# Kernel tuning notes

Measured on AMD Instinct MI355X. Metric: run time of the kernel, lower is better.

The kernel has to match this reference:

```python
import jax, jax.numpy as jnp
import numpy as np

# Production-scale dims (GraspNet-style CloudCrop)
B, N, C, NS = 8, 1024, 256, 32          # batch, seed points (= npoint), feat dim, nsample
RADIUS, HMIN, HMAX = 0.05, -0.02, 0.04
EPS = 1e-5


def setup_inputs() -> dict:
    key = jax.random.key(0)
    ks = jax.random.split(key, 8)
    # seed points in a 0.2m cube -> cylinder of r=0.05, h=0.06 holds ~60 pts on avg
    seed_xyz_graspable = jax.random.uniform(ks[0], (B, N, 3), dtype=jnp.float32) * 0.2
    seed_features_graspable = jax.random.normal(ks[1], (B, C, N), dtype=jnp.float32)
    # random proper-ish rotation matrices via batched QR (orthonormal columns)
    q, _ = jnp.linalg.qr(jax.random.normal(ks[2], (B, N, 3, 3), dtype=jnp.float32))
    vp_rot = q
    cin = 3 + C
    # kaiming_normal for 1x1 convs (fan_in = cin), BN -> no conv bias
    W1 = jax.random.normal(ks[3], (256, cin), dtype=jnp.float32) * np.sqrt(2.0 / cin)
    W2 = jax.random.normal(ks[4], (256, 256), dtype=jnp.float32) * np.sqrt(2.0 / 256)
    g1 = jnp.ones((256,), jnp.float32); b1 = jnp.zeros((256,), jnp.float32)
    g2 = jnp.ones((256,), jnp.float32); b2 = jnp.zeros((256,), jnp.float32)
    return dict(seed_xyz_graspable=seed_xyz_graspable,
                seed_features_graspable=seed_features_graspable,
                vp_rot=vp_rot, W1=W1, g1=g1, b1=b1, W2=W2, g2=g2, b2=b2)


def _cylinder_query_idx(xyz, new_xyz, rot):
    # local coords: x_rot = R^T (p - c); rot flattened row-major in the original,
    # so local_k = sum_m rot[m, k] * diff_m  ==  einsum(diff, rot)
    diff = xyz[:, None, :, :] - new_xyz[:, :, None, :]          # (B, P, N, 3)
    local = jnp.einsum('bpnm,bpmk->bpnk', diff, rot)            # (B, P, N, 3)
    d2 = local[..., 1] ** 2 + local[..., 2] ** 2
    mask = (d2 < RADIUS ** 2) & (local[..., 0] > HMIN) & (local[..., 0] < HMAX)
    # first NS in-cylinder indices in original point order; empty slots -> index 0
    order = jnp.argsort(~mask, axis=-1)[..., :NS]               # stable sort
    valid = jnp.take_along_axis(mask, order, axis=-1)
    return jnp.where(valid, order, 0)                           # (B, P, NS) int32


def _conv_bn_relu(x, W, g, b):
    # 1x1 conv as channel GEMM, BatchNorm2d (training stats), ReLU
    y = jnp.einsum('bcps,oc->bops', x, W)                       # (B, O, P, S)
    mu = y.mean(axis=(0, 2, 3), keepdims=True)
    var = y.var(axis=(0, 2, 3), keepdims=True)
    y = (y - mu) * jax.lax.rsqrt(var + EPS)
    y = y * g[None, :, None, None] + b[None, :, None, None]
    return jax.nn.relu(y)


def reference(seed_xyz_graspable, seed_features_graspable, vp_rot,
              W1, g1, b1, W2, g2, b2):
    xyz, feats, rot = seed_xyz_graspable, seed_features_graspable, vp_rot
    idx = _cylinder_query_idx(xyz, xyz, rot)                    # centers == seeds
    # group xyz: gather, recenter, normalize by radius, rotate into cylinder frame
    gx = jax.vmap(lambda p, i: p[i])(xyz, idx)                  # (B, P, NS, 3)
    gx = (gx - xyz[:, :, None, :]) / RADIUS
    gx = jnp.einsum('bpsm,bpmk->bpsk', gx, rot)                 # rotate_xyz
    gf = jax.vmap(lambda f, i: f[:, i])(feats, idx)             # (B, C, P, NS)
    x = jnp.concatenate([gx.transpose(0, 3, 1, 2), gf], axis=1)  # (B, 3+C, P, NS)
    x = _conv_bn_relu(x, W1, g1, b1)
    x = _conv_bn_relu(x, W2, g2, b2)
    return x.max(axis=-1)                                        # (B, 256, P)
```

## Files before the change

kernel.cpp:

```cpp
#include <hip/hip_runtime.h>
#include <hip/hip_bf16.h>

#define DB 8
#define DN 1024
#define DP 1024
#define DC 256
#define DNS 32
#define DBP (DB * DP)
#define K1 288
#define K2 256
#define XS 296
#define YS 258
#define ROWS 128
#define NG (DBP / 4)
#define NK1 (K1 / 32)
#define NK2 (K2 / 32)

constexpr float kRadius = 0.05f;
constexpr float kR2 = kRadius * kRadius;
constexpr float kHmin = -0.02f;
constexpr float kHmax = 0.04f;
constexpr float kEps = 1e-5f;
constexpr float kInvCnt = 1.0f / (float)(DB * DP * DNS);

typedef __bf16 bf16x8 __attribute__((ext_vector_type(8)));
typedef float f32x4 __attribute__((ext_vector_type(4)));
static_assert(sizeof(bf16x8) == 16, "bf16x8 must be 16B");
static_assert(ROWS * XS >= ROWS * YS, "y tile must fit in x_lds");

constexpr size_t OF_FEATST = 0;
constexpr size_t OF_W1B  = OF_FEATST + (size_t)DB * DN * DC / 2;
constexpr size_t OF_W2B  = OF_W1B + (size_t)DC * K1 / 2;
constexpr size_t OF_IDX  = OF_W2B + (size_t)DC * K2 / 2;
constexpr size_t OF_GX   = OF_IDX + (size_t)DBP * DNS;
constexpr size_t OF_PART = OF_GX + (size_t)DBP * DNS * 3;
constexpr size_t OF_YMAX = OF_PART + (size_t)DBP * DC * 2;
constexpr size_t OF_YMIN = OF_YMAX + (size_t)DBP * DC;
constexpr size_t OF_BN1  = OF_YMIN + (size_t)DBP * DC;
constexpr size_t OF_BN2  = OF_BN1 + 512;

__device__ inline ushort f2b(float x) {
  union { __hip_bfloat16 h; ushort u; } c;
  c.h = __float2bfloat16(x);
  return c.u;
}
__device__ inline float b2f(ushort u) {
  union { uint u; float f; } c;
  c.u = (uint)u << 16;
  return c.f;
}

__global__ void k_transpose_feats(const float* __restrict__ f, uint* __restrict__ ftb) {
  __shared__ float t[32][33];
  int ct = blockIdx.x, nt = blockIdx.y, b = blockIdx.z;
  int tx = threadIdx.x, ty = threadIdx.y;
#pragma unroll
  for (int k = 0; k < 4; ++k) {
    int c = ct * 32 + ty + k * 8;
    t[ty + k * 8][tx] = f[((size_t)b * DC + c) * DN + nt * 32 + tx];
  }
  __syncthreads();
  int tid = ty * 32 + tx;
  uint* dst = ftb + (size_t)b * DN * (DC / 2);
#pragma unroll
  for (int it = 0; it < 2; ++it) {
    int idx = it * 256 + tid;
    int nl = idx >> 4, cp = idx & 15;
    uint v = (uint)f2b(t[2 * cp][nl]) | ((uint)f2b(t[2 * cp + 1][nl]) << 16);
    dst[(size_t)(nt * 32 + nl) * (DC / 2) + ct * 16 + cp] = v;
  }
}

__global__ void k_prep_w1(const float* __restrict__ W1, ushort* __restrict__ W1b) {
  int gid = blockIdx.x * 256 + threadIdx.x;
  if (gid >= DC * K1) return;
  int o = gid / K1, kp = gid - o * K1;
  float v = 0.f;
  if (kp < 256) v = W1[o * 259 + 3 + kp];
  else if (kp < 259) v = W1[o * 259 + (kp - 256)];
  W1b[gid] = f2b(v);
}

__global__ void k_prep_w2(const float* __restrict__ W2, ushort* __restrict__ W2b) {
  int gid = blockIdx.x * 256 + threadIdx.x;
  if (gid >= DC * K2) return;
  W2b[gid] = f2b(W2[gid]);
}

__global__ void k_query(const float* __restrict__ xyz, const float* __restrict__ rot,
                        int* __restrict__ idxp, float* __restrict__ gxp) {
  int bp = blockIdx.x;
  int b = bp >> 10;
  int lane = threadIdx.x;
  __shared__ int sidx[DNS];
  __shared__ float srot[9], sc[3];
  if (lane < DNS) sidx[lane] = 0;
  if (lane < 9) srot[lane] = rot[(size_t)bp * 9 + lane];
  if (lane < 3) sc[lane] = xyz[(size_t)bp * 3 + lane];
  __syncthreads();
  float r00 = srot[0], r01 = srot[1], r02 = srot[2];
  float r10 = srot[3], r11 = srot[4], r12 = srot[5];
  float r20 = srot[6], r21 = srot[7], r22 = srot[8];
  float cx = sc[0], cy = sc[1], cz = sc[2];
  const float* xb = xyz + (size_t)b * DN * 3;
  int cnt = 0;
  for (int ch = 0; ch < DN / 64 && cnt < DNS; ++ch) {
    int n = ch * 64 + lane;
    float dx = xb[n * 3 + 0] - cx, dy = xb[n * 3 + 1] - cy, dz = xb[n * 3 + 2] - cz;
    float lx = dx * r00 + dy * r10 + dz * r20;
    float ly = dx * r01 + dy * r11 + dz * r21;
    float lz = dx * r02 + dy * r12 + dz * r22;
    bool m = (ly * ly + lz * lz < kR2) && (lx > kHmin) && (lx < kHmax);
    unsigned long long bal = __ballot(m);
    int rank = cnt + __popcll(bal & ((1ull << lane) - 1ull));
    if (m && rank < DNS) sidx[rank] = n;
    cnt += __popcll(bal);
  }
  __syncthreads();
  if (lane < DNS) {
    int j = sidx[lane];
    idxp[(size_t)bp * DNS + lane] = j;
    float gx = (xb[j * 3 + 0] - cx) / kRadius;
    float gy = (xb[j * 3 + 1] - cy) / kRadius;
    float gz = (xb[j * 3 + 2] - cz) / kRadius;
    float* gp = gxp + ((size_t)bp * DNS + lane) * 3;
    gp[0] = gx * r00 + gy * r10 + gz * r20;
    gp[1] = gx * r01 + gy * r11 + gz * r21;
    gp[2] = gx * r02 + gy * r12 + gz * r22;
  }
}

template <bool FULL>
__global__ __launch_bounds__(256, 2)
void k_gemm(const uint4* __restrict__ ftb, const ushort* __restrict__ W1b,
            const ushort* __restrict__ W2b, const int* __restrict__ idxp,
            const float* __restrict__ gxp, const float* __restrict__ bn1,
            float2* __restrict__ part, float* __restrict__ ymax,
            float* __restrict__ ymin) {
  __shared__ ushort x_lds[ROWS * XS];
  __shared__ float bn_lds[2 * DC];

  const int grp = blockIdx.x;
  const int bp0 = grp * 4;
  const int b = bp0 >> 10;
  const int tid = threadIdx.x;
  const int lane = tid & 63;
  const int wv = tid >> 6;
  const int l15 = lane & 15;
  const int l4 = lane >> 4;

  if constexpr (FULL) {
    for (int i = tid; i < 2 * DC; i += 256) bn_lds[i] = bn1[i];
  }

  {
    int q = tid & 7;
#pragma unroll
    for (int rep = 0; rep < 4; ++rep) {
      int s = (tid >> 3) + rep * 32;
      int j = idxp[(size_t)bp0 * DNS + s];
      const uint4* src = ftb + (size_t)(b * DN + j) * (DC / 8);
      uint4* dst = (uint4*)(x_lds + (size_t)s * XS);
#pragma unroll
      for (int k = 0; k < 4; ++k) dst[q + 8 * k] = src[q + 8 * k];
    }
  }
  if (tid < ROWS) {
    const float* g = gxp + ((size_t)bp0 * DNS + tid) * 3;
    uint a0 = (uint)f2b(g[0]) | ((uint)f2b(g[1]) << 16);
    uint a1 = (uint)f2b(g[2]);
    uint4* drow = (uint4*)(x_lds + (size_t)tid * XS + 256);
    drow[0] = make_uint4(a0, a1, 0u, 0u);
    drow[1] = make_uint4(0u, 0u, 0u, 0u);
    drow[2] = make_uint4(0u, 0u, 0u, 0u);
    drow[3] = make_uint4(0u, 0u, 0u, 0u);
  }
  __syncthreads();

  f32x4 acc[4][8];
#pragma unroll
  for (int t = 0; t < 4; ++t)
#pragma unroll
    for (int st = 0; st < 8; ++st)
#pragma unroll
      for (int r = 0; r < 4; ++r) acc[t][st][r] = 0.f;

  const int o0 = wv * 64;
  const ushort* xbase = x_lds + (size_t)l15 * XS + l4 * 8;

  {
    const ushort* wrow[4];
#pragma unroll
    for (int t = 0; t < 4; ++t)
      wrow[t] = W1b + (size_t)(o0 + t * 16 + l15) * K1 + l4 * 8;
    bf16x8 aw[4];
#pragma unroll
    for (int t = 0; t < 4; ++t) aw[t] = *(const bf16x8*)(wrow[t]);
#pragma unroll
    for (int ks = 0; ks < NK1; ++ks) {
      bf16x8 bx[8];
#pragma unroll
      for (int st = 0; st < 8; ++st)
        bx[st] = *(const bf16x8*)(xbase + (size_t)st * 16 * XS + ks * 32);
      bf16x8 an[4];
      if (ks + 1 < NK1) {
#pragma unroll
        for (int t = 0; t < 4; ++t)
          an[t] = *(const bf16x8*)(wrow[t] + (ks + 1) * 32);
      }
#pragma unroll
      for (int st = 0; st < 8; ++st)
#pragma unroll
        for (int t = 0; t < 4; ++t)
          acc[t][st] = __builtin_amdgcn_mfma_f32_16x16x32_bf16(aw[t], bx[st],
                                                               acc[t][st], 0, 0, 0);
      if (ks + 1 < NK1) {
#pragma unroll
        for (int t = 0; t < 4; ++t) aw[t] = an[t];
      }
    }
  }

  if constexpr (!FULL) {
    __syncthreads();
#pragma unroll
    for (int t = 0; t < 4; ++t) {
      int ob = o0 + t * 16 + l4 * 4;
#pragma unroll
      for (int st = 0; st < 8; ++st) {
        uint2 pk = make_uint2(
            (uint)f2b(acc[t][st][0]) | ((uint)f2b(acc[t][st][1]) << 16),
            (uint)f2b(acc[t][st][2]) | ((uint)f2b(acc[t][st][3]) << 16));
        int s = st * 16 + l15;
        *(uint2*)(x_lds + (size_t)s * YS + ob) = pk;
      }
    }
    __syncthreads();
    {
      const ushort* col = x_lds + tid;
      float s = 0.f, q = 0.f;
#pragma unroll 8
      for (int i = 0; i < ROWS; ++i) {
        float v = b2f(col[(size_t)i * YS]);
        s += v; q += v * v;
      }
      part[(size_t)grp * DC + tid] = make_float2(s, q);
    }
  } else {
    __syncthreads();
#pragma unroll
    for (int t = 0; t < 4; ++t) {
      int ob = o0 + t * 16 + l4 * 4;
      float sc0 = bn_lds[ob + 0], sh0 = bn_lds[DC + ob + 0];
      float sc1 = bn_lds[ob + 1], sh1 = bn_lds[DC + ob + 1];
      float sc2 = bn_lds[ob + 2], sh2 = bn_lds[DC + ob + 2];
      float sc3 = bn_lds[ob + 3], sh3 = bn_lds[DC + ob + 3];
#pragma unroll
      for (int st = 0; st < 8; ++st) {
        float v0 = fmaxf(fmaf(acc[t][st][0], sc0, sh0), 0.f);
        float v1 = fmaxf(fmaf(acc[t][st][1], sc1, sh1), 0.f);
        float v2 = fmaxf(fmaf(acc[t][st][2], sc2, sh2), 0.f);
        float v3 = fmaxf(fmaf(acc[t][st][3], sc3, sh3), 0.f);
        uint2 pk = make_uint2((uint)f2b(v0) | ((uint)f2b(v1) << 16),
                              (uint)f2b(v2) | ((uint)f2b(v3) << 16));
        int s = st * 16 + l15;
        *(uint2*)(x_lds + (size_t)s * XS + ob) = pk;
        acc[t][st][0] = 0.f; acc[t][st][1] = 0.f;
        acc[t][st][2] = 0.f; acc[t][st][3] = 0.f;
      }
    }
    __syncthreads();

    {
      const ushort* wrow[4];
#pragma unroll
      for (int t = 0; t < 4; ++t)
        wrow[t] = W2b + (size_t)(o0 + t * 16 + l15) * K2 + l4 * 8;
      bf16x8 aw[4];
#pragma unroll
      for (int t = 0; t < 4; ++t) aw[t] = *(const bf16x8*)(wrow[t]);
#pragma unroll
      for (int ks = 0; ks < NK2; ++ks) {
        bf16x8 bx[8];
#pragma unroll
        for (int st = 0; st < 8; ++st)
          bx[st] = *(const bf16x8*)(xbase + (size_t)st * 16 * XS + ks * 32);
        bf16x8 an[4];
        if (ks + 1 < NK2) {
#pragma unroll
          for (int t = 0; t < 4; ++t)
            an[t] = *(const bf16x8*)(wrow[t] + (ks + 1) * 32);
        }
#pragma unroll
        for (int st = 0; st < 8; ++st)
#pragma unroll
          for (int t = 0; t < 4; ++t)
            acc[t][st] = __builtin_amdgcn_mfma_f32_16x16x32_bf16(aw[t], bx[st],
                                                                 acc[t][st], 0, 0, 0);
        if (ks + 1 < NK2) {
#pragma unroll
          for (int t = 0; t < 4; ++t) aw[t] = an[t];
        }
      }
    }

    __syncthreads();
#pragma unroll
    for (int t = 0; t < 4; ++t) {
      int ob = o0 + t * 16 + l4 * 4;
#pragma unroll
      for (int st = 0; st < 8; ++st) {
        uint2 pk = make_uint2(
            (uint)f2b(acc[t][st][0]) | ((uint)f2b(acc[t][st][1]) << 16),
            (uint)f2b(acc[t][st][2]) | ((uint)f2b(acc[t][st][3]) << 16));
        int s = st * 16 + l15;
        *(uint2*)(x_lds + (size_t)s * YS + ob) = pk;
      }
    }
    __syncthreads();
    {
      const ushort* col = x_lds + tid;
      float s = 0.f, q = 0.f;
#pragma unroll
      for (int p = 0; p < 4; ++p) {
        float mx = -3.4e38f, mn = 3.4e38f;
#pragma unroll 8
        for (int i = 0; i < DNS; ++i) {
          float v = b2f(col[(size_t)(p * DNS + i) * YS]);
          s += v; q += v * v;
          mx = fmaxf(mx, v); mn = fminf(mn, v);
        }
        ymax[(size_t)(bp0 + p) * DC + tid] = mx;
        ymin[(size_t)(bp0 + p) * DC + tid] = mn;
      }
      part[(size_t)grp * DC + tid] = make_float2(s, q);
    }
  }
}

__global__ void k_reduce_bn(const float* __restrict__ part, const float* __restrict__ gam,
                            const float* __restrict__ bet, float* __restrict__ bn) {
  int o = blockIdx.x, tid = threadIdx.x;
  __shared__ float ss[256], sq[256];
  float s = 0.f, q = 0.f;
  const float2* pp = (const float2*)part;
  for (int g = tid; g < NG; g += 256) {
    float2 v = pp[(size_t)g * DC + o];
    s += v.x; q += v.y;
  }
  ss[tid] = s; sq[tid] = q;
  __syncthreads();
  for (int w = 128; w > 0; w >>= 1) {
    if (tid < w) { ss[tid] += ss[tid + w]; sq[tid] += sq[tid + w]; }
    __syncthreads();
  }
  if (tid == 0) {
    float mu = ss[0] * kInvCnt;
    float var = sq[0] * kInvCnt - mu * mu;
    var = var < 0.f ? 0.f : var;
    float sc = gam[o] * rsqrtf(var + kEps);
    bn[o] = sc;
    bn[DC + o] = bet[o] - mu * sc;
  }
}

__global__ void k_final(const float* __restrict__ ymax, const float* __restrict__ ymin,
                        const float* __restrict__ bn2, float* __restrict__ out) {
  __shared__ float tmax[32][33], tmin[32][33];
  int ot = blockIdx.x, pt = blockIdx.y, b = blockIdx.z;
  int tx = threadIdx.x, ty = threadIdx.y;
#pragma unroll
  for (int k = 0; k < 4; ++k) {
    int pr = ty + k * 8;
    size_t base = ((size_t)(b * DP) + pt * 32 + pr) * DC + ot * 32 + tx;
    tmax[pr][tx] = ymax[base];
    tmin[pr][tx] = ymin[base];
  }
  __syncthreads();
#pragma unroll
  for (int k = 0; k < 4; ++k) {
    int oc = ty + k * 8;
    int o = ot * 32 + oc;
    float sc = bn2[o], sh = bn2[DC + o];
    float m = (sc >= 0.f) ? tmax[tx][oc] : tmin[tx][oc];
    float v = fmaf(sc, m, sh);
    v = v > 0.f ? v : 0.f;
    out[((size_t)(b * DC) + o) * DP + pt * 32 + tx] = v;
  }
}

extern "C" void kernel_launch(void* const* d_in, const int* in_sizes, int n_in,
                              void* d_out, int out_size, void* d_ws, size_t ws_size,
                              hipStream_t stream) {
  const float* xyz   = (const float*)d_in[0];
  const float* feats = (const float*)d_in[1];
  const float* rot   = (const float*)d_in[2];
  const float* W1    = (const float*)d_in[3];
  const float* g1    = (const float*)d_in[4];
  const float* b1    = (const float*)d_in[5];
  const float* W2    = (const float*)d_in[6];
  const float* g2    = (const float*)d_in[7];
  const float* b2    = (const float*)d_in[8];
  float* out = (float*)d_out;

  float* ws = (float*)d_ws;
  uint*   ftb_u  = (uint*)(ws + OF_FEATST);
  uint4*  ftb    = (uint4*)(ws + OF_FEATST);
  ushort* W1b    = (ushort*)(ws + OF_W1B);
  ushort* W2b    = (ushort*)(ws + OF_W2B);
  int*    idxp   = (int*)(ws + OF_IDX);
  float*  gxp    = ws + OF_GX;
  float2* partp  = (float2*)(ws + OF_PART);
  float*  ymaxp  = ws + OF_YMAX;
  float*  yminp  = ws + OF_YMIN;
  float*  bn1p   = ws + OF_BN1;
  float*  bn2p   = ws + OF_BN2;

  k_transpose_feats<<<dim3(DC / 32, DN / 32, DB), dim3(32, 8), 0, stream>>>(feats, ftb_u);
  k_prep_w1<<<(DC * K1 + 255) / 256, 256, 0, stream>>>(W1, W1b);
  k_prep_w2<<<(DC * K2 + 255) / 256, 256, 0, stream>>>(W2, W2b);
  k_query<<<DBP, 64, 0, stream>>>(xyz, rot, idxp, gxp);

  k_gemm<false><<<NG, 256, 0, stream>>>(ftb, W1b, W2b, idxp, gxp, bn1p, partp,
                                        ymaxp, yminp);
  k_reduce_bn<<<DC, 256, 0, stream>>>((const float*)partp, g1, b1, bn1p);
  k_gemm<true><<<NG, 256, 0, stream>>>(ftb, W1b, W2b, idxp, gxp, bn1p, partp,
                                       ymaxp, yminp);
  k_reduce_bn<<<DC, 256, 0, stream>>>((const float*)partp, g2, b2, bn2p);
  k_final<<<dim3(DC / 32, DP / 32, DB), dim3(32, 8), 0, stream>>>(ymaxp, yminp, bn2p, out);
}
```

Before: 169.6 us.

## Compute BN1 statistics analytically from weighted feature Gram matrix instead of GEMM pass

Replaces the first full gathered GEMM pass, which existed only to gather BN1 sum and sum-of-squares, with an algebraic route. Per-point gather counts and summed local xyz are built with atomics, then a count-weighted second-moment matrix of the input channels is formed. BN1 mean and variance follow from W1 times that matrix times W1 transposed. This removes a whole pass of gather, MFMA and reduction over all 262k samples, at the cost of several small kernels, atomics and fp32 variance-by-subtraction precision risk.

```diff
diff --git a/kernel.cpp b/kernel.cpp
--- a/kernel.cpp
+++ b/kernel.cpp
@@ -26,7 +26,6 @@
 typedef __bf16 bf16x8 __attribute__((ext_vector_type(8)));
 typedef float f32x4 __attribute__((ext_vector_type(4)));
 static_assert(sizeof(bf16x8) == 16, "bf16x8 must be 16B");
-static_assert(ROWS * XS >= ROWS * YS, "y tile must fit in x_lds");
 
 constexpr size_t OF_FEATST = 0;
 constexpr size_t OF_W1B  = OF_FEATST + (size_t)DB * DN * DC / 2;
@@ -38,6 +37,11 @@
 constexpr size_t OF_YMIN = OF_YMAX + (size_t)DBP * DC;
 constexpr size_t OF_BN1  = OF_YMIN + (size_t)DBP * DC;
 constexpr size_t OF_BN2  = OF_BN1 + 512;
+constexpr size_t OF_CNT  = OF_BN2 + 512;
+constexpr size_t OF_GW   = OF_CNT + (size_t)DB * DN;
+constexpr size_t OF_GG   = OF_GW + (size_t)DB * 3 * DN;
+constexpr size_t OF_CM   = OF_GG + 16;
+constexpr int    ZN      = DB * DN + DB * 3 * DN + 16 + 257 * 259;
 
 __device__ inline ushort f2b(float x) {
   union { __hip_bfloat16 h; ushort u; } c;
@@ -130,13 +134,158 @@
   }
 }
 
-template <bool FULL>
+__global__ void k_zero(float* __restrict__ p, int n) {
+  int i = blockIdx.x * 256 + threadIdx.x;
+  if (i < n) p[i] = 0.f;
+}
+
+__global__ __launch_bounds__(256)
+void k_count(const int* __restrict__ idxp, const float* __restrict__ gxp,
+             float* __restrict__ cnt, float* __restrict__ gw, float* __restrict__ gg) {
+  int t = threadIdx.x;
+  float p[6] = {0.f, 0.f, 0.f, 0.f, 0.f, 0.f};
+#pragma unroll
+  for (int r = 0; r < 4; ++r) {
+    int sid = blockIdx.x * 1024 + r * 256 + t;
+    int b = sid >> 15;
+    int j = idxp[sid];
+    const float* g = gxp + (size_t)sid * 3;
+    float g0 = g[0], g1 = g[1], g2 = g[2];
+    atomicAdd(&cnt[b * DN + j], 1.f);
+    atomicAdd(&gw[(b * 3 + 0) * DN + j], g0);
+    atomicAdd(&gw[(b * 3 + 1) * DN + j], g1);
+    atomicAdd(&gw[(b * 3 + 2) * DN + j], g2);
+    p[0] += g0 * g0; p[1] += g0 * g1; p[2] += g0 * g2;
+    p[3] += g1 * g1; p[4] += g1 * g2; p[5] += g2 * g2;
+  }
+  __shared__ float sgg[4][6];
+#pragma unroll
+  for (int v = 0; v < 6; ++v) {
+    float s = p[v];
+#pragma unroll
+    for (int m = 1; m < 64; m <<= 1) s += __shfl_xor(s, m, 64);
+    if ((t & 63) == 0) sgg[t >> 6][v] = s;
+  }
+  __syncthreads();
+  if (t < 6) {
+    float s = sgg[0][t] + sgg[1][t] + sgg[2][t] + sgg[3][t];
+    const int i1[6] = {0, 1, 2, 4, 5, 8};
+    const int i2[6] = {0, 3, 6, 4, 7, 8};
+    atomicAdd(&gg[i1[t]], s);
+    if (i2[t] != i1[t]) atomicAdd(&gg[i2[t]], s);
+  }
+}
+
+__global__ __launch_bounds__(256)
+void k_xxt(const float* __restrict__ feats, const float* __restrict__ cnt,
+           const float* __restrict__ gw, float* __restrict__ Cm) {
+  __shared__ float As[16][65], Bs[16][65];
+  int bt = blockIdx.z >> 2;
+  int n0 = (blockIdx.z & 3) * 256;
+  int r0 = blockIdx.x * 64, c0 = blockIdx.y * 64;
+  int tid = threadIdx.x;
+  int ty = tid >> 4, tx = tid & 15;
+  int li = tid >> 2, lq = tid & 3;
+  const float* fb = feats + (size_t)bt * DC * DN;
+  const float* cb = cnt + (size_t)bt * DN;
+  const float* gb = gw + (size_t)bt * 3 * DN;
+  float acc[4][4];
+#pragma unroll
+  for (int u = 0; u < 4; ++u)
+#pragma unroll
+    for (int v = 0; v < 4; ++v) acc[u][v] = 0.f;
+
+  for (int nc = n0; nc < n0 + 256; nc += 16) {
+    __syncthreads();
+    {
+      int k1 = r0 + li;
+      float4 av = make_float4(0.f, 0.f, 0.f, 0.f);
+      if (k1 < 256) av = *(const float4*)(fb + (size_t)k1 * DN + nc + lq * 4);
+      else if (k1 == 256) av = make_float4(1.f, 1.f, 1.f, 1.f);
+      As[lq * 4 + 0][li] = av.x; As[lq * 4 + 1][li] = av.y;
+      As[lq * 4 + 2][li] = av.z; As[lq * 4 + 3][li] = av.w;
+      int k2 = c0 + li;
+      float4 bv = make_float4(0.f, 0.f, 0.f, 0.f);
+      if (k2 < 256) {
+        float4 f = *(const float4*)(fb + (size_t)k2 * DN + nc + lq * 4);
+        float4 c4 = *(const float4*)(cb + nc + lq * 4);
+        bv = make_float4(f.x * c4.x, f.y * c4.y, f.z * c4.z, f.w * c4.w);
+      } else if (k2 < 259) {
+        bv = *(const float4*)(gb + (size_t)(k2 - 256) * DN + nc + lq * 4);
+      }
+      Bs[lq * 4 + 0][li] = bv.x; Bs[lq * 4 + 1][li] = bv.y;
+      Bs[lq * 4 + 2][li] = bv.z; Bs[lq * 4 + 3][li] = bv.w;
+    }
+    __syncthreads();
+#pragma unroll
+    for (int kk = 0; kk < 16; ++kk) {
+      float a[4], bvv[4];
+#pragma unroll
+      for (int u = 0; u < 4; ++u) a[u] = As[kk][ty * 4 + u];
+#pragma unroll
+      for (int v = 0; v < 4; ++v) bvv[v] = Bs[kk][tx * 4 + v];
+#pragma unroll
+      for (int u = 0; u < 4; ++u)
+#pragma unroll
+        for (int v = 0; v < 4; ++v) acc[u][v] = fmaf(a[u], bvv[v], acc[u][v]);
+    }
+  }
+#pragma unroll
+  for (int u = 0; u < 4; ++u) {
+    int k1 = r0 + ty * 4 + u;
+    if (k1 > 256) continue;
+#pragma unroll
+    for (int v = 0; v < 4; ++v) {
+      int k2 = c0 + tx * 4 + v;
+      if (k2 < 259) atomicAdd(&Cm[(size_t)k1 * 259 + k2], acc[u][v]);
+    }
+  }
+}
+
+__global__ __launch_bounds__(256)
+void k_bn1(const float* __restrict__ Cm, const float* __restrict__ gg,
+           const float* __restrict__ W1, const float* __restrict__ gam,
+           const float* __restrict__ bet, float* __restrict__ bn) {
+  int o = blockIdx.x, t = threadIdx.x;
+  __shared__ float wv[259];
+  __shared__ float rq[256], rs[256];
+  for (int j = t; j < 259; j += 256)
+    wv[j] = (j < 256) ? W1[o * 259 + 3 + j] : W1[o * 259 + (j - 256)];
+  __syncthreads();
+  float qp = 0.f, sp = 0.f;
+  for (int j = t; j < 259; j += 256) {
+    float u = 0.f;
+    for (int i = 0; i < 256; ++i) u = fmaf(wv[i], Cm[(size_t)i * 259 + j], u);
+#pragma unroll
+    for (int c = 0; c < 3; ++c) {
+      float m = (j < 256) ? Cm[(size_t)j * 259 + 256 + c] : gg[c * 3 + (j - 256)];
+      u = fmaf(wv[256 + c], m, u);
+    }
+    qp = fmaf(wv[j], u, qp);
+    sp = fmaf(wv[j], Cm[(size_t)256 * 259 + j], sp);
+  }
+  rq[t] = qp; rs[t] = sp;
+  __syncthreads();
+  for (int w = 128; w > 0; w >>= 1) {
+    if (t < w) { rq[t] += rq[t + w]; rs[t] += rs[t + w]; }
+    __syncthreads();
+  }
+  if (t == 0) {
+    float mu = rs[0] * kInvCnt;
+    float var = rq[0] * kInvCnt - mu * mu;
+    var = var < 0.f ? 0.f : var;
+    float sc = gam[o] * rsqrtf(var + kEps);
+    bn[o] = sc;
+    bn[DC + o] = bet[o] - mu * sc;
+  }
+}
+
 __global__ __launch_bounds__(256, 2)
-void k_gemm(const uint4* __restrict__ ftb, const ushort* __restrict__ W1b,
-            const ushort* __restrict__ W2b, const int* __restrict__ idxp,
-            const float* __restrict__ gxp, const float* __restrict__ bn1,
-            float2* __restrict__ part, float* __restrict__ ymax,
-            float* __restrict__ ymin) {
+void k_gemm_full(const uint4* __restrict__ ftb, const ushort* __restrict__ W1b,
+                 const ushort* __restrict__ W2b, const int* __restrict__ idxp,
+                 const float* __restrict__ gxp, const float* __restrict__ bn1,
+                 float2* __restrict__ part, float* __restrict__ ymax,
+                 float* __restrict__ ymin) {
   __shared__ ushort x_lds[ROWS * XS];
   __shared__ float bn_lds[2 * DC];
 
@@ -149,9 +298,7 @@
   const int l15 = lane & 15;
   const int l4 = lane >> 4;
 
-  if constexpr (FULL) {
-    for (int i = tid; i < 2 * DC; i += 256) bn_lds[i] = bn1[i];
-  }
+  for (int i = tid; i < 2 * DC; i += 256) bn_lds[i] = bn1[i];
 
   {
     int q = tid & 7;
@@ -221,120 +368,93 @@
     }
   }
 
-  if constexpr (!FULL) {
-    __syncthreads();
-#pragma unroll
-    for (int t = 0; t < 4; ++t) {
-      int ob = o0 + t * 16 + l4 * 4;
-#pragma unroll
-      for (int st = 0; st < 8; ++st) {
-        uint2 pk = make_uint2(
-            (uint)f2b(acc[t][st][0]) | ((uint)f2b(acc[t][st][1]) << 16),
-            (uint)f2b(acc[t][st][2]) | ((uint)f2b(acc[t][st][3]) << 16));
-        int s = st * 16 + l15;
-        *(uint2*)(x_lds + (size_t)s * YS + ob) = pk;
+  __syncthreads();
+#pragma unroll
+  for (int t = 0; t < 4; ++t) {
+    int ob = o0 + t * 16 + l4 * 4;
+    float sc0 = bn_lds[ob + 0], sh0 = bn_lds[DC + ob + 0];
+    float sc1 = bn_lds[ob + 1], sh1 = bn_lds[DC + ob + 1];
+    float sc2 = bn_lds[ob + 2], sh2 = bn_lds[DC + ob + 2];
+    float sc3 = bn_lds[ob + 3], sh3 = bn_lds[DC + ob + 3];
+#pragma unroll
+    for (int st = 0; st < 8; ++st) {
+      float v0 = fmaxf(fmaf(acc[t][st][0], sc0, sh0), 0.f);
+      float v1 = fmaxf(fmaf(acc[t][st][1], sc1, sh1), 0.f);
+      float v2 = fmaxf(fmaf(acc[t][st][2], sc2, sh2), 0.f);
+      float v3 = fmaxf(fmaf(acc[t][st][3], sc3, sh3), 0.f);
+      uint2 pk = make_uint2((uint)f2b(v0) | ((uint)f2b(v1) << 16),
+                            (uint)f2b(v2) | ((uint)f2b(v3) << 16));
+      int s = st * 16 + l15;
+      *(uint2*)(x_lds + (size_t)s * XS + ob) = pk;
+      acc[t][st][0] = 0.f; acc[t][st][1] = 0.f;
+      acc[t][st][2] = 0.f; acc[t][st][3] = 0.f;
+    }
+  }
+  __syncthreads();
+
+  {
+    const ushort* wrow[4];
+#pragma unroll
+    for (int t = 0; t < 4; ++t)
+      wrow[t] = W2b + (size_t)(o0 + t * 16 + l15) * K2 + l4 * 8;
+    bf16x8 aw[4];
+#pragma unroll
+    for (int t = 0; t < 4; ++t) aw[t] = *(const bf16x8*)(wrow[t]);
+#pragma unroll
+    for (int ks = 0; ks < NK2; ++ks) {
+      bf16x8 bx[8];
+#pragma unroll
+      for (int st = 0; st < 8; ++st)
+        bx[st] = *(const bf16x8*)(xbase + (size_t)st * 16 * XS + ks * 32);
+      bf16x8 an[4];
+      if (ks + 1 < NK2) {
+#pragma unroll
+        for (int t = 0; t < 4; ++t)
+          an[t] = *(const bf16x8*)(wrow[t] + (ks + 1) * 32);
       }
-    }
-    __syncthreads();
-    {
-      const ushort* col = x_lds + tid;
-      float s = 0.f, q = 0.f;
+#pragma unroll
+      for (int st = 0; st < 8; ++st)
+#pragma unroll
+        for (int t = 0; t < 4; ++t)
+          acc[t][st] = __builtin_amdgcn_mfma_f32_16x16x32_bf16(aw[t], bx[st],
+                                                               acc[t][st], 0, 0, 0);
+      if (ks + 1 < NK2) {
+#pragma unroll
+        for (int t = 0; t < 4; ++t) aw[t] = an[t];
+      }
+    }
+  }
+
+  __syncthreads();
+#pragma unroll
+  for (int t = 0; t < 4; ++t) {
+    int ob = o0 + t * 16 + l4 * 4;
+#pragma unroll
+    for (int st = 0; st < 8; ++st) {
+      uint2 pk = make_uint2(
+          (uint)f2b(acc[t][st][0]) | ((uint)f2b(acc[t][st][1]) << 16),
+          (uint)f2b(acc[t][st][2]) | ((uint)f2b(acc[t][st][3]) << 16));
+      int s = st * 16 + l15;
+      *(uint2*)(x_lds + (size_t)s * YS + ob) = pk;
+    }
+  }
+  __syncthreads();
+  {
+    const ushort* col = x_lds + tid;
+    float s = 0.f, q = 0.f;
+#pragma unroll
+    for (int p = 0; p < 4; ++p) {
+      float mx = -3.4e38f, mn = 3.4e38f;
 #pragma unroll 8
-      for (int i = 0; i < ROWS; ++i) {
-        float v = b2f(col[(size_t)i * YS]);
+      for (int i = 0; i < DNS; ++i) {
+        float v = b2f(col[(size_t)(p * DNS + i) * YS]);
         s += v; q += v * v;
+        mx = fmaxf(mx, v); mn = fminf(mn, v);
       }
-      part[(size_t)grp * DC + tid] = make_float2(s, q);
-    }
-  } else {
-    __syncthreads();
-#pragma unroll
-    for (int t = 0; t < 4; ++t) {
-      int ob = o0 + t * 16 + l4 * 4;
-      float sc0 = bn_lds[ob + 0], sh0 = bn_lds[DC + ob + 0];
-      float sc1 = bn_lds[ob + 1], sh1 = bn_lds[DC + ob + 1];
-      float sc2 = bn_lds[ob + 2], sh2 = bn_lds[DC + ob + 2];
-      float sc3 = bn_lds[ob + 3], sh3 = bn_lds[DC + ob + 3];
-#pragma unroll
-      for (int st = 0; st < 8; ++st) {
-        float v0 = fmaxf(fmaf(acc[t][st][0], sc0, sh0), 0.f);
-        float v1 = fmaxf(fmaf(acc[t][st][1], sc1, sh1), 0.f);
-        float v2 = fmaxf(fmaf(acc[t][st][2], sc2, sh2), 0.f);
-        float v3 = fmaxf(fmaf(acc[t][st][3], sc3, sh3), 0.f);
-        uint2 pk = make_uint2((uint)f2b(v0) | ((uint)f2b(v1) << 16),
-                              (uint)f2b(v2) | ((uint)f2b(v3) << 16));
-        int s = st * 16 + l15;
-        *(uint2*)(x_lds + (size_t)s * XS + ob) = pk;
-        acc[t][st][0] = 0.f; acc[t][st][1] = 0.f;
-        acc[t][st][2] = 0.f; acc[t][st][3] = 0.f;
-      }
-    }
-    __syncthreads();
-
-    {
-      const ushort* wrow[4];
-#pragma unroll
-      for (int t = 0; t < 4; ++t)
-        wrow[t] = W2b + (size_t)(o0 + t * 16 + l15) * K2 + l4 * 8;
-      bf16x8 aw[4];
-#pragma unroll
-      for (int t = 0; t < 4; ++t) aw[t] = *(const bf16x8*)(wrow[t]);
-#pragma unroll
-      for (int ks = 0; ks < NK2; ++ks) {
-        bf16x8 bx[8];
-#pragma unroll
-        for (int st = 0; st < 8; ++st)
-          bx[st] = *(const bf16x8*)(xbase + (size_t)st * 16 * XS + ks * 32);
-        bf16x8 an[4];
-        if (ks + 1 < NK2) {
-#pragma unroll
-          for (int t = 0; t < 4; ++t)
-            an[t] = *(const bf16x8*)(wrow[t] + (ks + 1) * 32);
-        }
-#pragma unroll
-        for (int st = 0; st < 8; ++st)
-#pragma unroll
-          for (int t = 0; t < 4; ++t)
-            acc[t][st] = __builtin_amdgcn_mfma_f32_16x16x32_bf16(aw[t], bx[st],
-                                                                 acc[t][st], 0, 0, 0);
-        if (ks + 1 < NK2) {
-#pragma unroll
-          for (int t = 0; t < 4; ++t) aw[t] = an[t];
-        }
-      }
-    }
-
-    __syncthreads();
-#pragma unroll
-    for (int t = 0; t < 4; ++t) {
-      int ob = o0 + t * 16 + l4 * 4;
-#pragma unroll
-      for (int st = 0; st < 8; ++st) {
-        uint2 pk = make_uint2(
-            (uint)f2b(acc[t][st][0]) | ((uint)f2b(acc[t][st][1]) << 16),
-            (uint)f2b(acc[t][st][2]) | ((uint)f2b(acc[t][st][3]) << 16));
-        int s = st * 16 + l15;
-        *(uint2*)(x_lds + (size_t)s * YS + ob) = pk;
-      }
-    }
-    __syncthreads();
-    {
-      const ushort* col = x_lds + tid;
-      float s = 0.f, q = 0.f;
-#pragma unroll
-      for (int p = 0; p < 4; ++p) {
-        float mx = -3.4e38f, mn = 3.4e38f;
-#pragma unroll 8
-        for (int i = 0; i < DNS; ++i) {
-          float v = b2f(col[(size_t)(p * DNS + i) * YS]);
-          s += v; q += v * v;
-          mx = fmaxf(mx, v); mn = fminf(mn, v);
-        }
-        ymax[(size_t)(bp0 + p) * DC + tid] = mx;
-        ymin[(size_t)(bp0 + p) * DC + tid] = mn;
-      }
-      part[(size_t)grp * DC + tid] = make_float2(s, q);
-    }
+      ymax[(size_t)(bp0 + p) * DC + tid] = mx;
+      ymin[(size_t)(bp0 + p) * DC + tid] = mn;
+    }
+    part[(size_t)grp * DC + tid] = make_float2(s, q);
   }
 }
 
@@ -415,17 +535,23 @@
   float*  yminp  = ws + OF_YMIN;
   float*  bn1p   = ws + OF_BN1;
   float*  bn2p   = ws + OF_BN2;
+  float*  cntp   = ws + OF_CNT;
+  float*  gwp    = ws + OF_GW;
+  float*  ggp    = ws + OF_GG;
+  float*  cmp    = ws + OF_CM;
 
   k_transpose_feats<<<dim3(DC / 32, DN / 32, DB), dim3(32, 8), 0, stream>>>(feats, ftb_u);
   k_prep_w1<<<(DC * K1 + 255) / 256, 256, 0, stream>>>(W1, W1b);
   k_prep_w2<<<(DC * K2 + 255) / 256, 256, 0, stream>>>(W2, W2b);
   k_query<<<DBP, 64, 0, stream>>>(xyz, rot, idxp, gxp);
 
-  k_gemm<false><<<NG, 256, 0, stream>>>(ftb, W1b, W2b, idxp, gxp, bn1p, partp,
-                                        ymaxp, yminp);
-  k_reduce_bn<<<DC, 256, 0, stream>>>((const float*)partp, g1, b1, bn1p);
-  k_gemm<true><<<NG, 256, 0, stream>>>(ftb, W1b, W2b, idxp, gxp, bn1p, partp,
-                                       ymaxp, yminp);
+  k_zero<<<(ZN + 255) / 256, 256, 0, stream>>>(cntp, ZN);
+  k_count<<<DBP * DNS / 1024, 256, 0, stream>>>(idxp, gxp, cntp, gwp, ggp);
+  k_xxt<<<dim3(5, 5, 32), 256, 0, stream>>>(feats, cntp, gwp, cmp);
+  k_bn1<<<DC, 256, 0, stream>>>(cmp, ggp, W1, g1, b1, bn1p);
+
+  k_gemm_full<<<NG, 256, 0, stream>>>(ftb, W1b, W2b, idxp, gxp, bn1p, partp,
+                                      ymaxp, yminp);
   k_reduce_bn<<<DC, 256, 0, stream>>>((const float*)partp, g2, b2, bn2p);
   k_final<<<dim3(DC / 32, DP / 32, DB), dim3(32, 8), 0, stream>>>(ymaxp, yminp, bn2p, out);
 }
```

Measured after the change: 259.9 us. 1.53x slower.

## Compute BN1 statistics algebraically from point histograms instead of grouped GEMM pass

Applied to the files above, without the earlier changes.

Replaces the first full grouped GEMM pass used only for layer-1 BatchNorm statistics with an algebraic shortcut. Per-point multiplicity counts and gx sums are histogrammed, a small ungrouped GEMM over the 8K unique points gives W1·f, and the sums and sums of squares are rebuilt from count-weighted terms plus a 3x3 gx Gram matrix. This removes one of two 32x-redundant layer-1 GEMM passes over all grouped samples. It also merges the three prep kernels into one launch and adds s_setprio around MFMA blocks. The stats now come from fp32 accumulators rather than bf16-rounded values, and the single-block BN1 reduction and 64-block ygemm underuse the GPU.

```diff
diff --git a/kernel.cpp b/kernel.cpp
--- a/kernel.cpp
+++ b/kernel.cpp
@@ -26,7 +26,6 @@
 typedef __bf16 bf16x8 __attribute__((ext_vector_type(8)));
 typedef float f32x4 __attribute__((ext_vector_type(4)));
 static_assert(sizeof(bf16x8) == 16, "bf16x8 must be 16B");
-static_assert(ROWS * XS >= ROWS * YS, "y tile must fit in x_lds");
 
 constexpr size_t OF_FEATST = 0;
 constexpr size_t OF_W1B  = OF_FEATST + (size_t)DB * DN * DC / 2;
@@ -38,6 +37,10 @@
 constexpr size_t OF_YMIN = OF_YMAX + (size_t)DBP * DC;
 constexpr size_t OF_BN1  = OF_YMIN + (size_t)DBP * DC;
 constexpr size_t OF_BN2  = OF_BN1 + 512;
+constexpr size_t OF_CNTZ = OF_BN2 + 512;
+constexpr size_t OF_GWZ  = OF_CNTZ + (size_t)64 * DN;
+constexpr size_t OF_GG64 = OF_GWZ + (size_t)64 * 3 * DN;
+constexpr size_t OF_YPRT = OF_GG64 + 512;
 
 __device__ inline ushort f2b(float x) {
   union { __hip_bfloat16 h; ushort u; } c;
@@ -50,41 +53,43 @@
   return c.f;
 }
 
-__global__ void k_transpose_feats(const float* __restrict__ f, uint* __restrict__ ftb) {
+__global__ __launch_bounds__(256)
+void k_prep(const float* __restrict__ f, uint* __restrict__ ftb,
+            const float* __restrict__ W1, ushort* __restrict__ W1b,
+            const float* __restrict__ W2, ushort* __restrict__ W2b) {
   __shared__ float t[32][33];
-  int ct = blockIdx.x, nt = blockIdx.y, b = blockIdx.z;
-  int tx = threadIdx.x, ty = threadIdx.y;
-#pragma unroll
-  for (int k = 0; k < 4; ++k) {
-    int c = ct * 32 + ty + k * 8;
-    t[ty + k * 8][tx] = f[((size_t)b * DC + c) * DN + nt * 32 + tx];
-  }
-  __syncthreads();
-  int tid = ty * 32 + tx;
-  uint* dst = ftb + (size_t)b * DN * (DC / 2);
-#pragma unroll
-  for (int it = 0; it < 2; ++it) {
-    int idx = it * 256 + tid;
-    int nl = idx >> 4, cp = idx & 15;
-    uint v = (uint)f2b(t[2 * cp][nl]) | ((uint)f2b(t[2 * cp + 1][nl]) << 16);
-    dst[(size_t)(nt * 32 + nl) * (DC / 2) + ct * 16 + cp] = v;
-  }
-}
-
-__global__ void k_prep_w1(const float* __restrict__ W1, ushort* __restrict__ W1b) {
-  int gid = blockIdx.x * 256 + threadIdx.x;
-  if (gid >= DC * K1) return;
-  int o = gid / K1, kp = gid - o * K1;
-  float v = 0.f;
-  if (kp < 256) v = W1[o * 259 + 3 + kp];
-  else if (kp < 259) v = W1[o * 259 + (kp - 256)];
-  W1b[gid] = f2b(v);
-}
-
-__global__ void k_prep_w2(const float* __restrict__ W2, ushort* __restrict__ W2b) {
-  int gid = blockIdx.x * 256 + threadIdx.x;
-  if (gid >= DC * K2) return;
-  W2b[gid] = f2b(W2[gid]);
+  int blk = blockIdx.x;
+  int tid = threadIdx.x;
+  if (blk < 2048) {
+    int ct = blk & 7, nt = (blk >> 3) & 31, b = blk >> 8;
+    int tx = tid & 31, ty = tid >> 5;
+#pragma unroll
+    for (int k = 0; k < 4; ++k) {
+      int c = ct * 32 + ty + k * 8;
+      t[ty + k * 8][tx] = f[((size_t)b * DC + c) * DN + nt * 32 + tx];
+    }
+    __syncthreads();
+    uint* dst = ftb + (size_t)b * DN * (DC / 2);
+#pragma unroll
+    for (int it = 0; it < 2; ++it) {
+      int idx = it * 256 + tid;
+      int nl = idx >> 4, cp = idx & 15;
+      uint v = (uint)f2b(t[2 * cp][nl]) | ((uint)f2b(t[2 * cp + 1][nl]) << 16);
+      dst[(size_t)(nt * 32 + nl) * (DC / 2) + ct * 16 + cp] = v;
+    }
+  } else if (blk < 2336) {
+    int gid = (blk - 2048) * 256 + tid;
+    if (gid < DC * K1) {
+      int o = gid / K1, kp = gid - o * K1;
+      float v = 0.f;
+      if (kp < 256) v = W1[o * 259 + 3 + kp];
+      else if (kp < 259) v = W1[o * 259 + (kp - 256)];
+      W1b[gid] = f2b(v);
+    }
+  } else {
+    int gid = (blk - 2336) * 256 + tid;
+    if (gid < DC * K2) W2b[gid] = f2b(W2[gid]);
+  }
 }
 
 __global__ void k_query(const float* __restrict__ xyz, const float* __restrict__ rot,
@@ -130,13 +135,208 @@
   }
 }
 
-template <bool FULL>
+__global__ __launch_bounds__(256)
+void k_count(const int* __restrict__ idxp, const float* __restrict__ gxp,
+             float* __restrict__ cntz, float* __restrict__ gwz,
+             float* __restrict__ gg64) {
+  __shared__ float h0[DN], h1[DN], h2[DN], h3[DN];
+  int t = threadIdx.x;
+  int blk = blockIdx.x;
+  int b = blk >> 3, s = blk & 7;
+  for (int i = t; i < DN; i += 256) {
+    h0[i] = 0.f; h1[i] = 0.f; h2[i] = 0.f; h3[i] = 0.f;
+  }
+  __syncthreads();
+  float p[6] = {0.f, 0.f, 0.f, 0.f, 0.f, 0.f};
+#pragma unroll
+  for (int r = 0; r < 16; ++r) {
+    int sid = blk * 4096 + r * 256 + t;
+    int j = idxp[sid];
+    const float* g = gxp + (size_t)sid * 3;
+    float g0 = g[0], g1 = g[1], g2 = g[2];
+    atomicAdd(&h0[j], 1.f);
+    atomicAdd(&h1[j], g0);
+    atomicAdd(&h2[j], g1);
+    atomicAdd(&h3[j], g2);
+    p[0] += g0 * g0; p[1] += g0 * g1; p[2] += g0 * g2;
+    p[3] += g1 * g1; p[4] += g1 * g2; p[5] += g2 * g2;
+  }
+  __syncthreads();
+  for (int i = t; i < DN; i += 256) {
+    cntz[((size_t)b * 8 + s) * DN + i] = h0[i];
+    gwz[(((size_t)b * 8 + s) * 3 + 0) * DN + i] = h1[i];
+    gwz[(((size_t)b * 8 + s) * 3 + 1) * DN + i] = h2[i];
+    gwz[(((size_t)b * 8 + s) * 3 + 2) * DN + i] = h3[i];
+  }
+  __shared__ float sgg[4][6];
+#pragma unroll
+  for (int v = 0; v < 6; ++v) {
+    float sv = p[v];
+#pragma unroll
+    for (int m = 1; m < 64; m <<= 1) sv += __shfl_xor(sv, m, 64);
+    if ((t & 63) == 0) sgg[t >> 6][v] = sv;
+  }
+  __syncthreads();
+  if (t < 6) gg64[blk * 8 + t] = sgg[0][t] + sgg[1][t] + sgg[2][t] + sgg[3][t];
+}
+
+__global__ __launch_bounds__(256)
+void k_ygemm(const uint4* __restrict__ ftb, const ushort* __restrict__ W1b,
+             const float* __restrict__ W1, const float* __restrict__ cntz,
+             const float* __restrict__ gwz, float2* __restrict__ ypart) {
+  __shared__ ushort x_lds[ROWS * XS];
+  __shared__ float c_lds[ROWS];
+  __shared__ float g_lds[3][ROWS];
+  __shared__ float wg_lds[DC][3];
+
+  const int nb = blockIdx.x;
+  const int b = nb >> 3;
+  const int n0 = (nb & 7) * ROWS;
+  const int tid = threadIdx.x;
+  const int lane = tid & 63;
+  const int wv = tid >> 6;
+  const int l15 = lane & 15;
+  const int l4 = lane >> 4;
+
+  {
+    const uint4* src = ftb + ((size_t)b * DN + n0) * (DC / 8);
+    for (int idx = tid; idx < ROWS * 32; idx += 256) {
+      int rrow = idx >> 5, col = idx & 31;
+      ((uint4*)(x_lds + (size_t)rrow * XS))[col] = src[rrow * 32 + col];
+    }
+  }
+  if (tid < ROWS) {
+    float c = 0.f, g0 = 0.f, g1 = 0.f, g2 = 0.f;
+#pragma unroll
+    for (int s = 0; s < 8; ++s) {
+      c += cntz[((size_t)b * 8 + s) * DN + n0 + tid];
+      g0 += gwz[(((size_t)b * 8 + s) * 3 + 0) * DN + n0 + tid];
+      g1 += gwz[(((size_t)b * 8 + s) * 3 + 1) * DN + n0 + tid];
+      g2 += gwz[(((size_t)b * 8 + s) * 3 + 2) * DN + n0 + tid];
+    }
+    c_lds[tid] = c; g_lds[0][tid] = g0; g_lds[1][tid] = g1; g_lds[2][tid] = g2;
+  }
+  {
+    wg_lds[tid][0] = W1[tid * 259 + 0];
+    wg_lds[tid][1] = W1[tid * 259 + 1];
+    wg_lds[tid][2] = W1[tid * 259 + 2];
+  }
+  __syncthreads();
+
+  f32x4 acc[4][8];
+#pragma unroll
+  for (int t = 0; t < 4; ++t)
+#pragma unroll
+    for (int st = 0; st < 8; ++st)
+#pragma unroll
+      for (int r = 0; r < 4; ++r) acc[t][st][r] = 0.f;
+
+  const int o0 = wv * 64;
+  const ushort* xbase = x_lds + (size_t)l15 * XS + l4 * 8;
+  {
+    const ushort* wrow[4];
+#pragma unroll
+    for (int t = 0; t < 4; ++t)
+      wrow[t] = W1b + (size_t)(o0 + t * 16 + l15) * K1 + l4 * 8;
+#pragma unroll
+    for (int ks = 0; ks < 8; ++ks) {
+      bf16x8 bx[8], aw[4];
+#pragma unroll
+      for (int st = 0; st < 8; ++st)
+        bx[st] = *(const bf16x8*)(xbase + (size_t)st * 16 * XS + ks * 32);
+#pragma unroll
+      for (int t = 0; t < 4; ++t) aw[t] = *(const bf16x8*)(wrow[t] + ks * 32);
+#pragma unroll
+      for (int st = 0; st < 8; ++st)
+#pragma unroll
+        for (int t = 0; t < 4; ++t)
+          acc[t][st] = __builtin_amdgcn_mfma_f32_16x16x32_bf16(aw[t], bx[st],
+                                                               acc[t][st], 0, 0, 0);
+    }
+  }
+
+  float cn[8], h0[8], h1[8], h2[8];
+#pragma unroll
+  for (int st = 0; st < 8; ++st) {
+    int n = st * 16 + l15;
+    cn[st] = c_lds[n]; h0[st] = g_lds[0][n]; h1[st] = g_lds[1][n]; h2[st] = g_lds[2][n];
+  }
+#pragma unroll
+  for (int t = 0; t < 4; ++t) {
+#pragma unroll
+    for (int r = 0; r < 4; ++r) {
+      int o = o0 + t * 16 + l4 * 4 + r;
+      float wg0 = wg_lds[o][0], wg1 = wg_lds[o][1], wg2 = wg_lds[o][2];
+      float s = 0.f, q = 0.f;
+#pragma unroll
+      for (int st = 0; st < 8; ++st) {
+        float Y = acc[t][st][r];
+        float h = wg0 * h0[st] + wg1 * h1[st] + wg2 * h2[st];
+        s = fmaf(cn[st], Y, s);
+        q += cn[st] * Y * Y + 2.f * Y * h;
+      }
+#pragma unroll
+      for (int m = 1; m < 16; m <<= 1) {
+        s += __shfl_xor(s, m, 64);
+        q += __shfl_xor(q, m, 64);
+      }
+      if (l15 == 0) ypart[(size_t)nb * DC + o] = make_float2(s, q);
+    }
+  }
+}
+
+__global__ __launch_bounds__(256)
+void k_bn1f(const float2* __restrict__ ypart, const float* __restrict__ gwz,
+            const float* __restrict__ gg64, const float* __restrict__ W1,
+            const float* __restrict__ gam, const float* __restrict__ bet,
+            float* __restrict__ bn) {
+  __shared__ float red[256];
+  __shared__ float gtot[3], ggs[6];
+  int t = threadIdx.x;
+  for (int c = 0; c < 3; ++c) {
+    float s = 0.f;
+    for (int idx = t; idx < 64 * DN; idx += 256) {
+      int bs = idx >> 10, n = idx & (DN - 1);
+      s += gwz[((size_t)bs * 3 + c) * DN + n];
+    }
+    red[t] = s;
+    __syncthreads();
+    for (int w = 128; w > 0; w >>= 1) {
+      if (t < w) red[t] += red[t + w];
+      __syncthreads();
+    }
+    if (t == 0) gtot[c] = red[0];
+    __syncthreads();
+  }
+  if (t < 6) {
+    float s = 0.f;
+    for (int blk = 0; blk < 64; ++blk) s += gg64[blk * 8 + t];
+    ggs[t] = s;
+  }
+  __syncthreads();
+  float s = 0.f, q = 0.f;
+  for (int nb = 0; nb < 64; ++nb) {
+    float2 v = ypart[(size_t)nb * DC + t];
+    s += v.x; q += v.y;
+  }
+  float wg0 = W1[t * 259 + 0], wg1 = W1[t * 259 + 1], wg2 = W1[t * 259 + 2];
+  s += wg0 * gtot[0] + wg1 * gtot[1] + wg2 * gtot[2];
+  q += wg0 * wg0 * ggs[0] + 2.f * wg0 * wg1 * ggs[1] + 2.f * wg0 * wg2 * ggs[2] +
+       wg1 * wg1 * ggs[3] + 2.f * wg1 * wg2 * ggs[4] + wg2 * wg2 * ggs[5];
+  float mu = s * kInvCnt;
+  float var = q * kInvCnt - mu * mu;
+  var = var < 0.f ? 0.f : var;
+  float sc = gam[t] * rsqrtf(var + kEps);
+  bn[t] = sc;
+  bn[DC + t] = bet[t] - mu * sc;
+}
+
 __global__ __launch_bounds__(256, 2)
-void k_gemm(const uint4* __restrict__ ftb, const ushort* __restrict__ W1b,
-            const ushort* __restrict__ W2b, const int* __restrict__ idxp,
-            const float* __restrict__ gxp, const float* __restrict__ bn1,
-            float2* __restrict__ part, float* __restrict__ ymax,
-            float* __restrict__ ymin) {
+void k_gemm_full(const uint4* __restrict__ ftb, const ushort* __restrict__ W1b,
+                 const ushort* __restrict__ W2b, const int* __restrict__ idxp,
+                 const float* __restrict__ gxp, const float* __restrict__ bn1,
+                 float2* __restrict__ part, float* __restrict__ ymax,
+                 float* __restrict__ ymin) {
   __shared__ ushort x_lds[ROWS * XS];
   __shared__ float bn_lds[2 * DC];
 
@@ -149,9 +349,7 @@
   const int l15 = lane & 15;
   const int l4 = lane >> 4;
 
-  if constexpr (FULL) {
-    for (int i = tid; i < 2 * DC; i += 256) bn_lds[i] = bn1[i];
-  }
+  for (int i = tid; i < 2 * DC; i += 256) bn_lds[i] = bn1[i];
 
   {
     int q = tid & 7;
@@ -208,12 +406,14 @@
         for (int t = 0; t < 4; ++t)
           an[t] = *(const bf16x8*)(wrow[t] + (ks + 1) * 32);
       }
+      __builtin_amdgcn_s_setprio(1);
 #pragma unroll
       for (int st = 0; st < 8; ++st)
 #pragma unroll
         for (int t = 0; t < 4; ++t)
           acc[t][st] = __builtin_amdgcn_mfma_f32_16x16x32_bf16(aw[t], bx[st],
                                                                acc[t][st], 0, 0, 0);
+      __builtin_amdgcn_s_setprio(0);
       if (ks + 1 < NK1) {
 #pragma unroll
         for (int t = 0; t < 4; ++t) aw[t] = an[t];
@@ -221,120 +421,95 @@
     }
   }
 
-  if constexpr (!FULL) {
-    __syncthreads();
-#pragma unroll
-    for (int t = 0; t < 4; ++t) {
-      int ob = o0 + t * 16 + l4 * 4;
-#pragma unroll
-      for (int st = 0; st < 8; ++st) {
-        uint2 pk = make_uint2(
-            (uint)f2b(acc[t][st][0]) | ((uint)f2b(acc[t][st][1]) << 16),
-            (uint)f2b(acc[t][st][2]) | ((uint)f2b(acc[t][st][3]) << 16));
-        int s = st * 16 + l15;
-        *(uint2*)(x_lds + (size_t)s * YS + ob) = pk;
+  __syncthreads();
+#pragma unroll
+  for (int t = 0; t < 4; ++t) {
+    int ob = o0 + t * 16 + l4 * 4;
+    float sc0 = bn_lds[ob + 0], sh0 = bn_lds[DC + ob + 0];
+    float sc1 = bn_lds[ob + 1], sh1 = bn_lds[DC + ob + 1];
+    float sc2 = bn_lds[ob + 2], sh2 = bn_lds[DC + ob + 2];
+    float sc3 = bn_lds[ob + 3], sh3 = bn_lds[DC + ob + 3];
+#pragma unroll
+    for (int st = 0; st < 8; ++st) {
+      float v0 = fmaxf(fmaf(acc[t][st][0], sc0, sh0), 0.f);
+      float v1 = fmaxf(fmaf(acc[t][st][1], sc1, sh1), 0.f);
+      float v2 = fmaxf(fmaf(acc[t][st][2], sc2, sh2), 0.f);
+      float v3 = fmaxf(fmaf(acc[t][st][3], sc3, sh3), 0.f);
+      uint2 pk = make_uint2((uint)f2b(v0) | ((uint)f2b(v1) << 16),
+                            (uint)f2b(v2) | ((uint)f2b(v3) << 16));
+      int s = st * 16 + l15;
+      *(uint2*)(x_lds + (size_t)s * XS + ob) = pk;
+      acc[t][st][0] = 0.f; acc[t][st][1] = 0.f;
+      acc[t][st][2] = 0.f; acc[t][st][3] = 0.f;
+    }
+  }
+  __syncthreads();
+
+  {
+    const ushort* wrow[4];
+#pragma unroll
+    for (int t = 0; t < 4; ++t)
+      wrow[t] = W2b + (size_t)(o0 + t * 16 + l15) * K2 + l4 * 8;
+    bf16x8 aw[4];
+#pragma unroll
+    for (int t = 0; t < 4; ++t) aw[t] = *(const bf16x8*)(wrow[t]);
+#pragma unroll
+    for (int ks = 0; ks < NK2; ++ks) {
+      bf16x8 bx[8];
+#pragma unroll
+      for (int st = 0; st < 8; ++st)
+        bx[st] = *(const bf16x8*)(xbase + (size_t)st * 16 * XS + ks * 32);
+      bf16x8 an[4];
+      if (ks + 1 < NK2) {
+#pragma unroll
+        for (int t = 0; t < 4; ++t)
+          an[t] = *(const bf16x8*)(wrow[t] + (ks + 1) * 32);
       }
-    }
-    __syncthreads();
-    {
-      const ushort* col = x_lds + tid;
-      float s = 0.f, q = 0.f;
+      __builtin_amdgcn_s_setprio(1);
+#pragma unroll
+      for (int st = 0; st < 8; ++st)
+#pragma unroll
+        for (int t = 0; t < 4; ++t)
+          acc[t][st] = __builtin_amdgcn_mfma_f32_16x16x32_bf16(aw[t], bx[st],
+                                                               acc[t][st], 0, 0, 0);
+      __builtin_amdgcn_s_setprio(0);
+      if (ks + 1 < NK2) {
+#pragma unroll
+        for (int t = 0; t < 4; ++t) aw[t] = an[t];
+      }
+    }
+  }
+
+  __syncthreads();
+#pragma unroll
+  for (int t = 0; t < 4; ++t) {
+    int ob = o0 + t * 16 + l4 * 4;
+#pragma unroll
+    for (int st = 0; st < 8; ++st) {
+      uint2 pk = make_uint2(
+          (uint)f2b(acc[t][st][0]) | ((uint)f2b(acc[t][st][1]) << 16),
+          (uint)f2b(acc[t][st][2]) | ((uint)f2b(acc[t][st][3]) << 16));
+      int s = st * 16 + l15;
+      *(uint2*)(x_lds + (size_t)s * YS + ob) = pk;
+    }
+  }
+  __syncthreads();
+  {
+    const ushort* col = x_lds + tid;
+    float s = 0.f, q = 0.f;
+#pragma unroll
+    for (int p = 0; p < 4; ++p) {
+      float mx = -3.4e38f, mn = 3.4e38f;
 #pragma unroll 8
-      for (int i = 0; i < ROWS; ++i) {
-        float v = b2f(col[(size_t)i * YS]);
+      for (int i = 0; i < DNS; ++i) {
+        float v = b2f(col[(size_t)(p * DNS + i) * YS]);
         s += v; q += v * v;
+        mx = fmaxf(mx, v); mn = fminf(mn, v);
       }
-      part[(size_t)grp * DC + tid] = make_float2(s, q);
-    }
-  } else {
-    __syncthreads();
-#pragma unroll
-    for (int t = 0; t < 4; ++t) {
-      int ob = o0 + t * 16 + l4 * 4;
-      float sc0 = bn_lds[ob + 0], sh0 = bn_lds[DC + ob + 0];
-      float sc1 = bn_lds[ob + 1], sh1 = bn_lds[DC + ob + 1];
-      float sc2 = bn_lds[ob + 2], sh2 = bn_lds[DC + ob + 2];
-      float sc3 = bn_lds[ob + 3], sh3 = bn_lds[DC + ob + 3];
-#pragma unroll
-      for (int st = 0; st < 8; ++st) {
-        float v0 = fmaxf(fmaf(acc[t][st][0], sc0, sh0), 0.f);
-        float v1 = fmaxf(fmaf(acc[t][st][1], sc1, sh1), 0.f);
-        float v2 = fmaxf(fmaf(acc[t][st][2], sc2, sh2), 0.f);
-        float v3 = fmaxf(fmaf(acc[t][st][3], sc3, sh3), 0.f);
-        uint2 pk = make_uint2((uint)f2b(v0) | ((uint)f2b(v1) << 16),
-                              (uint)f2b(v2) | ((uint)f2b(v3) << 16));
-        int s = st * 16 + l15;
-        *(uint2*)(x_lds + (size_t)s * XS + ob) = pk;
-        acc[t][st][0] = 0.f; acc[t][st][1] = 0.f;
-        acc[t][st][2] = 0.f; acc[t][st][3] = 0.f;
-      }
-    }
-    __syncthreads();
-
-    {
-      const ushort* wrow[4];
-#pragma unroll
-      for (int t = 0; t < 4; ++t)
-        wrow[t] = W2b + (size_t)(o0 + t * 16 + l15) * K2 + l4 * 8;
-      bf16x8 aw[4];
-#pragma unroll
-      for (int t = 0; t < 4; ++t) aw[t] = *(const bf16x8*)(wrow[t]);
-#pragma unroll
-      for (int ks = 0; ks < NK2; ++ks) {
-        bf16x8 bx[8];
-#pragma unroll
-        for (int st = 0; st < 8; ++st)
-          bx[st] = *(const bf16x8*)(xbase + (size_t)st * 16 * XS + ks * 32);
-        bf16x8 an[4];
-        if (ks + 1 < NK2) {
-#pragma unroll
-          for (int t = 0; t < 4; ++t)
-            an[t] = *(const bf16x8*)(wrow[t] + (ks + 1) * 32);
-        }
-#pragma unroll
-        for (int st = 0; st < 8; ++st)
-#pragma unroll
-          for (int t = 0; t < 4; ++t)
-            acc[t][st] = __builtin_amdgcn_mfma_f32_16x16x32_bf16(aw[t], bx[st],
-                                                                 acc[t][st], 0, 0, 0);
-        if (ks + 1 < NK2) {
-#pragma unroll
-          for (int t = 0; t < 4; ++t) aw[t] = an[t];
-        }
-      }
-    }
-
-    __syncthreads();
-#pragma unroll
-    for (int t = 0; t < 4; ++t) {
-      int ob = o0 + t * 16 + l4 * 4;
-#pragma unroll
-      for (int st = 0; st < 8; ++st) {
-        uint2 pk = make_uint2(
-            (uint)f2b(acc[t][st][0]) | ((uint)f2b(acc[t][st][1]) << 16),
-            (uint)f2b(acc[t][st][2]) | ((uint)f2b(acc[t][st][3]) << 16));
-        int s = st * 16 + l15;
-        *(uint2*)(x_lds + (size_t)s * YS + ob) = pk;
-      }
-    }
-    __syncthreads();
-    {
-      const ushort* col = x_lds + tid;
-      float s = 0.f, q = 0.f;
-#pragma unroll
-      for (int p = 0; p < 4; ++p) {
-        float mx = -3.4e38f, mn = 3.4e38f;
-#pragma unroll 8
-        for (int i = 0; i < DNS; ++i) {
-          float v = b2f(col[(size_t)(p * DNS + i) * YS]);
-          s += v; q += v * v;
-          mx = fmaxf(mx, v); mn = fminf(mn, v);
-        }
-        ymax[(size_t)(bp0 + p) * DC + tid] = mx;
-        ymin[(size_t)(bp0 + p) * DC + tid] = mn;
-      }
-      part[(size_t)grp * DC + tid] = make_float2(s, q);
-    }
+      ymax[(size_t)(bp0 + p) * DC + tid] = mx;
+      ymin[(size_t)(bp0 + p) * DC + tid] = mn;
+    }
+    part[(size_t)grp * DC + tid] = make_float2(s, q);
   }
 }
 
@@ -415,17 +590,20 @@
   float*  yminp  = ws + OF_YMIN;
   float*  bn1p   = ws + OF_BN1;
   float*  bn2p   = ws + OF_BN2;
-
-  k_transpose_feats<<<dim3(DC / 32, DN / 32, DB), dim3(32, 8), 0, stream>>>(feats, ftb_u);
-  k_prep_w1<<<(DC * K1 + 255) / 256, 256, 0, stream>>>(W1, W1b);
-  k_prep_w2<<<(DC * K2 + 255) / 256, 256, 0, stream>>>(W2, W2b);
+  float*  cntzp  = ws + OF_CNTZ;
+  float*  gwzp   = ws + OF_GWZ;
+  float*  gg64p  = ws + OF_GG64;
+  float2* yprtp  = (float2*)(ws + OF_YPRT);
+
+  k_prep<<<2592, 256, 0, stream>>>(feats, ftb_u, W1, W1b, W2, W2b);
   k_query<<<DBP, 64, 0, stream>>>(xyz, rot, idxp, gxp);
 
-  k_gemm<false><<<NG, 256, 0, stream>>>(ftb, W1b, W2b, idxp, gxp, bn1p, partp,
-                                        ymaxp, yminp);
-  k_reduce_bn<<<DC, 256, 0, stream>>>((const float*)partp, g1, b1, bn1p);
-  k_gemm<true><<<NG, 256, 0, stream>>>(ftb, W1b, W2b, idxp, gxp, bn1p, partp,
-                                       ymaxp, yminp);
+  k_count<<<64, 256, 0, stream>>>(idxp, gxp, cntzp, gwzp, gg64p);
+  k_ygemm<<<64, 256, 0, stream>>>(ftb, W1b, W1, cntzp, gwzp, yprtp);
+  k_bn1f<<<1, 256, 0, stream>>>(yprtp, gwzp, gg64p, W1, g1, b1, bn1p);
+
+  k_gemm_full<<<NG, 256, 0, stream>>>(ftb, W1b, W2b, idxp, gxp, bn1p, partp,
+                                      ymaxp, yminp);
   k_reduce_bn<<<DC, 256, 0, stream>>>((const float*)partp, g2, b2, bn2p);
   k_final<<<dim3(DC / 32, DP / 32, DB), dim3(32, 8), 0, stream>>>(ymaxp, yminp, bn2p, out);
 }
```

Result: slower. 360.6 us (+112.5%).
